# Kernel tuning notes

Measured on AMD Instinct MI355X. Metric: run time of the kernel, lower is better.

## Reference

```python
import jax, jax.numpy as jnp
import numpy as np
from jax import lax

DIM = 512
HEADS = 8
N = 2048
B = 4
EPS = 1e-12  # torch F.normalize eps


def setup_inputs() -> dict:
    key = jax.random.key(0)
    ks = jax.random.split(key, 8)
    s = 0.02
    return {
        "x": jax.random.normal(ks[0], (B, DIM, N), jnp.float32),
        "w_qkv": jax.random.normal(ks[1], (3 * DIM, DIM, 1), jnp.float32) * s,
        "b_qkv": jax.random.normal(ks[2], (3 * DIM,), jnp.float32) * s,
        "w_dw": jax.random.normal(ks[3], (3 * DIM, 1, 3), jnp.float32) * s,
        "b_dw": jax.random.normal(ks[4], (3 * DIM,), jnp.float32) * s,
        "w_po": jax.random.normal(ks[5], (DIM, DIM, 1), jnp.float32) * s,
        "b_po": jax.random.normal(ks[6], (DIM,), jnp.float32) * s,
        "temperature": jnp.ones((HEADS, 1, 1), jnp.float32),
    }


def _l2norm(x, axis):
    n = jnp.sqrt(jnp.sum(x * x, axis=axis, keepdims=True))
    return x / jnp.maximum(n, EPS)


def reference(x, w_qkv, b_qkv, w_dw, b_dw, w_po, b_po, temperature):
    b, c, n = x.shape
    ch = c // HEADS
    # 1x1 conv (pointwise)
    qkv = jnp.einsum('oc,bcn->bon', w_qkv[:, :, 0], x) + b_qkv[None, :, None]
    # depthwise conv k=3, pad=1
    qkv = lax.conv_general_dilated(
        qkv, w_dw, window_strides=(1,), padding=[(1, 1)],
        dimension_numbers=('NCH', 'OIH', 'NCH'),
        feature_group_count=3 * c) + b_dw[None, :, None]
    q, k, v = jnp.split(qkv, 3, axis=1)  # each [b, c, n]
    q = q.reshape(b, HEADS, ch, n)
    k = k.reshape(b, HEADS, ch, n)
    v = v.reshape(b, HEADS, ch, n)
    q = _l2norm(q, axis=-1)          # normalize over sequence axis
    k = _l2norm(k, axis=1)           # normalize over HEAD axis (faithful)
    # attn[i, j] = sum_c k[c, i] * q[c, j]  -> [b, h, n, n]
    attn = jnp.einsum('bhci,bhcj->bhij', k, q) * temperature[None]
    attn = jax.nn.softmax(attn, axis=-1)
    out = jnp.einsum('bhij,bhcj->bhic', attn, v)  # [b, h, n, ch]
    out = out.transpose(0, 1, 3, 2).reshape(b, c, n)  # b (head c) n
    out = jnp.einsum('oc,bcn->bon', w_po[:, :, 0], out) + b_po[None, :, None]
    return out
```

## Files before the change

kernel.cpp:

```cpp
#include <hip/hip_runtime.h>
#include <hip/hip_bf16.h>

#define BATCH 4
#define DIM 512
#define HEADS 8
#define CH 64
#define SEQ 2048
#define C3 1536
#define L2EPS 1e-12f

typedef float f32x4 __attribute__((ext_vector_type(4)));
typedef short s16x8 __attribute__((ext_vector_type(8)));
typedef unsigned short ushort_t;

static __device__ __forceinline__ unsigned bfpair(float a, float b) {
  unsigned ua = __builtin_bit_cast(unsigned, a);
  unsigned ub = __builtin_bit_cast(unsigned, b);
  ua = (ua + 0x7FFFu + ((ua >> 16) & 1u)) >> 16;
  ub = (ub + 0x7FFFu + ((ub >> 16) & 1u)) >> 16;
  return ua | (ub << 16);
}

static __device__ __forceinline__ ushort_t bf16r(float a) {
  unsigned u = __builtin_bit_cast(unsigned, a);
  u = (u + 0x7FFFu + ((u >> 16) & 1u)) >> 16;
  return (ushort_t)u;
}

static __device__ __forceinline__ float bf2f(ushort_t u) {
  return __builtin_bit_cast(float, ((unsigned)u) << 16);
}

static __device__ __forceinline__ unsigned cvtpk(float lo, float hi) {
  unsigned r;
  asm("v_cvt_pk_bf16_f32 %0, %1, %2" : "=v"(r) : "v"(lo), "v"(hi));
  return r;
}

static __device__ __forceinline__ float fexp2(float x) {
  float r;
  asm("v_exp_f32 %0, %1" : "=v"(r) : "v"(x));
  return r;
}

static __device__ __forceinline__ void gl_lds16(const void* g, void* l) {
  __builtin_amdgcn_global_load_lds(
      (const __attribute__((address_space(1))) unsigned int*)g,
      (__attribute__((address_space(3))) unsigned int*)l, 16, 0, 0);
}

__global__ __launch_bounds__(256) void prep_inputs(
    const float* __restrict__ x, const float* __restrict__ wq,
    const float* __restrict__ wp, unsigned* __restrict__ xbt,
    unsigned* __restrict__ wqb, unsigned* __restrict__ wpb) {
  __shared__ unsigned T[64][32];
  const int bid = blockIdx.x;
  if (bid < 1024) {
    const int xx = bid & 31, ky = (bid >> 5) & 7, b = bid >> 8;
    const int k0 = ky * 64;
    const int n0 = xx * 64;
    const int nl = threadIdx.x & 63;
    const int dwg = threadIdx.x >> 6;
    const float* xb = x + ((size_t)b * DIM + k0) * SEQ + n0 + nl;
#pragma unroll
    for (int dd = 0; dd < 8; ++dd) {
      const int dw = dwg * 8 + dd;
      const float v0 = xb[(size_t)(2 * dw) * SEQ];
      const float v1 = xb[(size_t)(2 * dw + 1) * SEQ];
      T[nl][dw ^ (4 * (nl & 7))] = bfpair(v0, v1);
    }
    __syncthreads();
#pragma unroll
    for (int rep = 0; rep < 8; ++rep) {
      const int id = rep * 256 + threadIdx.x;
      const int row = id >> 5, dw = id & 31;
      xbt[((size_t)b * SEQ + n0 + row) * 256 + (k0 >> 1) + dw] = T[row][dw];
    }
  } else {
    const int id = (bid - 1024) * 256 + threadIdx.x;
    const float* src;
    unsigned* dst;
    int rid;
    if (id < 1536 * 256) { src = wq; dst = wqb; rid = id; }
    else                 { src = wp; dst = wpb; rid = id - 1536 * 256; }
    const int m = rid >> 8, dcol = rid & 255;
    const int chunk = dcol >> 5, dw = dcol & 31;
    const int sdw = chunk * 32 + (dw ^ (4 * (m & 7)));
    const float* s = src + (size_t)m * 512 + 2 * sdw;
    dst[rid] = bfpair(s[0], s[1]);
  }
}

template <bool OBF, int BM>
__global__ __launch_bounds__(256) void gemm_mfma_bf16(
    const ushort_t* __restrict__ Wb, const ushort_t* __restrict__ Bt,
    const float* __restrict__ bias, float* __restrict__ Y,
    int M, int N) {
  constexpr int AW = BM / 4;
  constexpr int MFR = BM / 32;
  __shared__ __align__(16) char lds[BM * 128 + 16384];
  char* As = lds;
  char* Bs = lds + BM * 128;
  const int b = blockIdx.z;
  const int m0 = blockIdx.y * BM, n0 = blockIdx.x * 128;
  const int t = threadIdx.x, w = t >> 6, lane = t & 63;
  const int l15 = lane & 15, g = lane >> 4;
  const int key = 16 * (l15 & 7);
  const int wm = (w >> 1) * (BM / 2), wn = (w & 1) * 64;

  const int rsub = lane >> 3;
  const int csub = (lane & 7) * 8;

  f32x4 acc[MFR][4] = {};

  const ushort_t* Ag0 = Wb + (size_t)(m0 + AW * w + rsub) * 512 + csub;
  const ushort_t* Bg0 = Bt + ((size_t)b * N + n0 + 32 * w + rsub) * 512 + csub;
  char* Al0 = As + (AW * w) * 128;
  char* Bl0 = Bs + (32 * w) * 128;

  for (int kc = 0; kc < 8; ++kc) {
    const int ko64 = kc * 64;
#pragma unroll
    for (int ri = 0; ri < 4; ++ri) {
      if (ri < AW / 8)
        gl_lds16(Ag0 + (size_t)(8 * ri) * 512 + ko64, Al0 + ri * 1024);
      gl_lds16(Bg0 + (size_t)(8 * ri) * 512 + ko64, Bl0 + ri * 1024);
    }
    __syncthreads();
    const char* Abase = As + (wm + l15) * 128;
    const char* Bbase = Bs + (wn + l15) * 128;
#pragma unroll
    for (int ks = 0; ks < 2; ++ks) {
      const int ko = (64 * ks + 16 * g) ^ key;
      s16x8 af[MFR], bf[4];
#pragma unroll
      for (int mf = 0; mf < MFR; ++mf) af[mf] = *(const s16x8*)(Abase + mf * 2048 + ko);
#pragma unroll
      for (int nf = 0; nf < 4; ++nf) bf[nf] = *(const s16x8*)(Bbase + nf * 2048 + ko);
#pragma unroll
      for (int mf = 0; mf < MFR; ++mf)
#pragma unroll
        for (int nf = 0; nf < 4; ++nf)
          acc[mf][nf] = __builtin_amdgcn_mfma_f32_16x16x32_bf16(
              af[mf], bf[nf], acc[mf][nf], 0, 0, 0);
    }
    __syncthreads();
  }

#pragma unroll
  for (int mf = 0; mf < MFR; ++mf) {
#pragma unroll
    for (int rg = 0; rg < 4; ++rg) {
      const int m = m0 + wm + 16 * mf + 4 * g + rg;
      const float bv = bias[m];
      if constexpr (OBF) {
        ushort_t* yp =
            (ushort_t*)Y + ((size_t)b * M + m) * N + n0 + wn + l15;
#pragma unroll
        for (int nf = 0; nf < 4; ++nf)
          yp[16 * nf] = bf16r(acc[mf][nf][rg] + bv);
      } else {
        float* yp = Y + ((size_t)b * M + m) * N + n0 + wn + l15;
#pragma unroll
        for (int nf = 0; nf < 4; ++nf)
          yp[16 * nf] = acc[mf][nf][rg] + bv;
      }
    }
  }
}

__global__ __launch_bounds__(256) void dwconv2(
    const ushort_t* __restrict__ pre, const float* __restrict__ wdw,
    const float* __restrict__ bdw, ushort_t* __restrict__ qkv,
    unsigned* __restrict__ vb, float* __restrict__ rq) {
  __shared__ float red[4];
  const int row = blockIdx.x;
  const int o = row % C3;
  const int b = row / C3;
  const int n0 = threadIdx.x * 8;
  const ushort_t* src = pre + (size_t)row * SEQ + n0;
  const s16x8 mv = *(const s16x8*)src;
  const float left  = (n0 > 0) ? bf2f(src[-1]) : 0.f;
  const float right = (n0 < SEQ - 8) ? bf2f(src[8]) : 0.f;
  const float w0 = wdw[o * 3 + 0], w1 = wdw[o * 3 + 1], w2 = wdw[o * 3 + 2];
  const float bv = bdw[o];
  float mid[8];
#pragma unroll
  for (int u = 0; u < 8; ++u) mid[u] = bf2f((ushort_t)mv[u]);
  const float lf[8] = {left,   mid[0], mid[1], mid[2],
                       mid[3], mid[4], mid[5], mid[6]};
  const float rt[8] = {mid[1], mid[2], mid[3], mid[4],
                       mid[5], mid[6], mid[7], right};
  float y[8];
#pragma unroll
  for (int u = 0; u < 8; ++u) y[u] = w0 * lf[u] + w1 * mid[u] + w2 * rt[u] + bv;

  if (o < 2 * DIM) {
    uint4 pk;
    pk.x = bfpair(y[0], y[1]); pk.y = bfpair(y[2], y[3]);
    pk.z = bfpair(y[4], y[5]); pk.w = bfpair(y[6], y[7]);
    *(uint4*)(qkv + (size_t)row * SEQ + n0) = pk;
    if (o < DIM) {
      float s = 0.f;
#pragma unroll
      for (int u = 0; u < 8; ++u) s += y[u] * y[u];
#pragma unroll
      for (int off = 32; off > 0; off >>= 1) s += __shfl_down(s, off);
      if ((threadIdx.x & 63) == 0) red[threadIdx.x >> 6] = s;
      __syncthreads();
      if (threadIdx.x == 0) {
        const float tv = red[0] + red[1] + red[2] + red[3];
        rq[b * DIM + o] = 1.0f / fmaxf(sqrtf(tv), L2EPS);
      }
    }
  } else {
    const int oc = o - 2 * DIM;
    const int h = oc >> 6, cc = oc & 63;
    const int bh = b * 8 + h;
    const int jt = n0 >> 6, d0 = (n0 & 63) >> 1;
    uint4 pk;
    pk.x = bfpair(y[0], y[1]); pk.y = bfpair(y[2], y[3]);
    pk.z = bfpair(y[4], y[5]); pk.w = bfpair(y[6], y[7]);
    *(uint4*)&vb[((size_t)(bh * 32 + jt) * 64 + cc) * 32 +
                 (d0 ^ (4 * (cc & 7)))] = pk;
  }
}

__global__ __launch_bounds__(256) void knorm_kernel(
    const ushort_t* __restrict__ qkv, float* __restrict__ rk) {
  const int idx = blockIdx.x * 256 + threadIdx.x;
  const int n = idx & (SEQ - 1);
  const int cc = (idx >> 11) & 63;
  const int b = idx >> 17;
  const ushort_t* base = qkv + ((size_t)b * C3 + DIM + cc) * SEQ + n;
  float s = 0.f;
#pragma unroll
  for (int h = 0; h < HEADS; ++h) {
    float v = bf2f(base[(size_t)h * CH * SEQ]);
    s += v * v;
  }
  rk[idx] = 1.0f / fmaxf(sqrtf(s), L2EPS);
}

__global__ __launch_bounds__(256) void prep2(
    const ushort_t* __restrict__ qkv, const float* __restrict__ rq,
    const float* __restrict__ rk, const float* __restrict__ temp,
    unsigned* __restrict__ qt, unsigned* __restrict__ kt) {
  __shared__ unsigned T[64][32];
  const int jt = blockIdx.x, bh = blockIdx.y, sec = blockIdx.z;
  const int b = bh >> 3, h = bh & 7;
  const int jl = threadIdx.x & 63, dwg = threadIdx.x >> 6;
  const int j = jt * 64 + jl;
  if (sec == 0) {
    const ushort_t* base = qkv + ((size_t)b * C3 + h * CH) * SEQ + j;
    const float* rqb = rq + b * DIM + h * CH;
#pragma unroll
    for (int dd = 0; dd < 8; ++dd) {
      const int dw = dwg * 8 + dd;
      float v0 = bf2f(base[(size_t)(2 * dw) * SEQ]) * rqb[2 * dw];
      float v1 = bf2f(base[(size_t)(2 * dw + 1) * SEQ]) * rqb[2 * dw + 1];
      T[jl][dw ^ (4 * (jl & 7))] = bfpair(v0, v1);
    }
  } else {
    const float f = temp[h] * 1.44269504f;
    const ushort_t* base = qkv + ((size_t)b * C3 + DIM + h * CH) * SEQ + j;
    const float* rkb = rk + (size_t)b * CH * SEQ + j;
#pragma unroll
    for (int dd = 0; dd < 8; ++dd) {
      const int dw = dwg * 8 + dd;
      float v0 = bf2f(base[(size_t)(2 * dw) * SEQ]) *
                 rkb[(size_t)(2 * dw) * SEQ] * f;
      float v1 = bf2f(base[(size_t)(2 * dw + 1) * SEQ]) *
                 rkb[(size_t)(2 * dw + 1) * SEQ] * f;
      T[jl][dw ^ (4 * (jl & 7))] = bfpair(v0, v1);
    }
  }
  __syncthreads();
  unsigned* dst = (sec == 0 ? qt : kt) + ((size_t)bh * SEQ + jt * 64) * 32;
#pragma unroll
  for (int rep = 0; rep < 8; ++rep) {
    const int id = rep * 256 + threadIdx.x;
    const int row = id >> 5, dw = id & 31;
    const unsigned val = T[row][dw ^ (4 * (row & 7))];
    if (sec == 0) {
      const int s = row >> 5, rl = row & 31;
      const int dr = (s << 5) | (16 * ((rl >> 2) & 1) + 4 * (rl >> 3) + (rl & 3));
      dst[dr * 32 + (dw ^ (4 * (dr & 7)))] = val;
    } else {
      dst[row * 32 + dw] = val;
    }
  }
}

__global__ __launch_bounds__(256, 2) void flash_mfma(
    const ushort_t* __restrict__ qt, const ushort_t* __restrict__ kt,
    const ushort_t* __restrict__ vb, unsigned* __restrict__ attn_t) {
  __shared__ __align__(16) char lds[65536];
  char* const QA = lds;
  char* const QB = lds + 16384;
  char* const VA = lds + 32768;
  char* const VB = lds + 49152;

  const int orig = blockIdx.y * 16 + blockIdx.x;
  const int swz = (orig & 7) * 64 + (orig >> 3);
  const int bh = swz >> 4, b = bh >> 3, h = bh & 7;
  const int i0 = (swz & 15) * 128;

  const int t = threadIdx.x, w = t >> 6, lane = t & 63;
  const int l15 = lane & 15, g = lane >> 4;
  const int key = 16 * (lane & 7);

  const ushort_t* ktp =
      kt + ((size_t)bh * SEQ + i0 + 32 * w + l15) * 64 + 8 * g;
  s16x8 kf0[2], kf1[2];
#pragma unroll
  for (int ib = 0; ib < 2; ++ib) {
    kf0[ib] = *(const s16x8*)(ktp + ib * 1024);
    kf1[ib] = *(const s16x8*)(ktp + ib * 1024 + 32);
  }

  const ushort_t* qtile = qt + (size_t)bh * SEQ * 64;
  const ushort_t* vtile = vb + (size_t)bh * 32 * 4096;

  const int li0 = (w * 2) * 64 + lane;
  const int li1 = li0 + 64;
  const int wo = (w * 2) * 1024;

  f32x4 accO[4][2] = {};
  float lr[2] = {};

#define FSTAGE2(JT, QD, VD)                                               \
  do {                                                                    \
    gl_lds16(qtile + (size_t)(JT) * 4096 + li0 * 8, (QD) + wo);           \
    gl_lds16(qtile + (size_t)(JT) * 4096 + li1 * 8, (QD) + wo + 1024);    \
    gl_lds16(qtile + (size_t)(JT + 1) * 4096 + li0 * 8, (QD) + 8192 + wo);\
    gl_lds16(qtile + (size_t)(JT + 1) * 4096 + li1 * 8,                   \
             (QD) + 8192 + wo + 1024);                                    \
    gl_lds16(vtile + (size_t)(JT) * 4096 + li0 * 8, (VD) + wo);           \
    gl_lds16(vtile + (size_t)(JT) * 4096 + li1 * 8, (VD) + wo + 1024);    \
    gl_lds16(vtile + (size_t)(JT + 1) * 4096 + li0 * 8, (VD) + 8192 + wo);\
    gl_lds16(vtile + (size_t)(JT + 1) * 4096 + li1 * 8,                   \
             (VD) + 8192 + wo + 1024);                                    \
  } while (0)

  auto compute = [&](const char* Qs, const char* Vs) {
    s16x8 vf[2][4];
#pragma unroll
    for (int ks = 0; ks < 2; ++ks)
#pragma unroll
      for (int mf = 0; mf < 4; ++mf)
        vf[ks][mf] = *(const s16x8*)(Vs + (16 * mf + l15) * 128 +
                                     ((16 * g + 64 * ks) ^ key));

    f32x4 st[4][2];
    __builtin_amdgcn_s_setprio(1);
#pragma unroll
    for (int jf = 0; jf < 4; ++jf) {
      const char* qrow = Qs + (16 * jf + l15) * 128;
      s16x8 a0 = *(const s16x8*)(qrow + ((16 * g) ^ key));
      s16x8 a1 = *(const s16x8*)(qrow + ((16 * g + 64) ^ key));
#pragma unroll
      for (int ib = 0; ib < 2; ++ib) {
        f32x4 z = {};
        z = __builtin_amdgcn_mfma_f32_16x16x32_bf16(a0, kf0[ib], z, 0, 0, 0);
        z = __builtin_amdgcn_mfma_f32_16x16x32_bf16(a1, kf1[ib], z, 0, 0, 0);
        st[jf][ib] = z;
      }
    }
    __builtin_amdgcn_s_setprio(0);

    s16x8 pb[2][2];
#pragma unroll
    for (int ib = 0; ib < 2; ++ib)
#pragma unroll
      for (int ks = 0; ks < 2; ++ks) {
        const float e0 = fexp2(st[2 * ks][ib][0]);
        const float e1 = fexp2(st[2 * ks][ib][1]);
        const float e2 = fexp2(st[2 * ks][ib][2]);
        const float e3 = fexp2(st[2 * ks][ib][3]);
        const float e4 = fexp2(st[2 * ks + 1][ib][0]);
        const float e5 = fexp2(st[2 * ks + 1][ib][1]);
        const float e6 = fexp2(st[2 * ks + 1][ib][2]);
        const float e7 = fexp2(st[2 * ks + 1][ib][3]);
        lr[ib] += ((e0 + e1) + (e2 + e3)) + ((e4 + e5) + (e6 + e7));
        uint4 u;
        u.x = cvtpk(e0, e1);
        u.y = cvtpk(e2, e3);
        u.z = cvtpk(e4, e5);
        u.w = cvtpk(e6, e7);
        pb[ib][ks] = __builtin_bit_cast(s16x8, u);
      }

    __builtin_amdgcn_s_setprio(1);
#pragma unroll
    for (int ks = 0; ks < 2; ++ks)
#pragma unroll
      for (int mf = 0; mf < 4; ++mf)
#pragma unroll
        for (int ib = 0; ib < 2; ++ib)
          accO[mf][ib] = __builtin_amdgcn_mfma_f32_16x16x32_bf16(
              vf[ks][mf], pb[ib][ks], accO[mf][ib], 0, 0, 0);
    __builtin_amdgcn_s_setprio(0);
  };

  FSTAGE2(0, QA, VA);
  __syncthreads();
#pragma unroll 1
  for (int s = 0; s < 8; ++s) {
    const int t4 = 4 * s;
    FSTAGE2(t4 + 2, QB, VB);
    compute(QA, VA);
    compute(QA + 8192, VA + 8192);
    __syncthreads();
    if (s < 7) FSTAGE2(t4 + 4, QA, VA);
    compute(QB, VB);
    compute(QB + 8192, VB + 8192);
    __syncthreads();
  }

  float inv[2];
#pragma unroll
  for (int ib = 0; ib < 2; ++ib) {
    lr[ib] += __shfl_xor(lr[ib], 16);
    lr[ib] += __shfl_xor(lr[ib], 32);
    inv[ib] = 1.0f / lr[ib];
  }

  unsigned* Pw = (unsigned*)(lds + w * 4096);
  const int kk = 4 * (l15 & 7);
#pragma unroll
  for (int ib = 0; ib < 2; ++ib)
#pragma unroll
    for (int mf = 0; mf < 4; ++mf) {
      uint2 pk;
      pk.x = cvtpk(accO[mf][ib][0] * inv[ib], accO[mf][ib][1] * inv[ib]);
      pk.y = cvtpk(accO[mf][ib][2] * inv[ib], accO[mf][ib][3] * inv[ib]);
      const int dwb = 8 * mf + 2 * g;
      *(uint2*)&Pw[(16 * ib + l15) * 32 + (dwb ^ kk)] = pk;
    }
  __syncthreads();
#pragma unroll
  for (int rep = 0; rep < 16; ++rep) {
    const int id = rep * 64 + lane;
    const int row = id >> 5, dw = id & 31;
    attn_t[((size_t)b * SEQ + i0 + 32 * w + row) * 256 + h * 32 + dw] =
        Pw[row * 32 + dw];
  }
#undef FSTAGE2
}

extern "C" void kernel_launch(void* const* d_in, const int* in_sizes, int n_in,
                              void* d_out, int out_size, void* d_ws, size_t ws_size,
                              hipStream_t stream) {
  const float* x      = (const float*)d_in[0];
  const float* w_qkv  = (const float*)d_in[1];
  const float* b_qkv  = (const float*)d_in[2];
  const float* w_dw   = (const float*)d_in[3];
  const float* b_dw   = (const float*)d_in[4];
  const float* w_po   = (const float*)d_in[5];
  const float* b_po   = (const float*)d_in[6];
  const float* temp   = (const float*)d_in[7];
  float* out = (float*)d_out;
  float* ws  = (float*)d_ws;

  ushort_t* qkv_pre_b = (ushort_t*)ws;
  ushort_t* qkvb = (ushort_t*)(ws + 12582912);
  float* rq      = ws + 25165824;
  float* rk      = ws + 25167872;
  unsigned* xbt  = (unsigned*)(ws + 25692160);
  unsigned* wqb  = (unsigned*)(ws + 27789312);
  unsigned* wpb  = (unsigned*)(ws + 28182528);
  unsigned* vb     = (unsigned*)(ws + 25692160);
  unsigned* qt     = (unsigned*)(ws);
  unsigned* kt     = (unsigned*)(ws + 2097152);
  unsigned* attn_t = (unsigned*)(ws + 4194304);

  prep_inputs<<<3072, 256, 0, stream>>>(x, w_qkv, w_po, xbt, wqb, wpb);

  gemm_mfma_bf16<true, 128>
      <<<dim3(SEQ / 128, C3 / 128, BATCH), 256, 0, stream>>>(
          (const ushort_t*)wqb, (const ushort_t*)xbt, b_qkv,
          (float*)qkv_pre_b, C3, SEQ);

  dwconv2<<<BATCH * C3, 256, 0, stream>>>(qkv_pre_b, w_dw, b_dw, qkvb, vb, rq);

  knorm_kernel<<<(BATCH * CH * SEQ) / 256, 256, 0, stream>>>(qkvb, rk);

  prep2<<<dim3(32, BATCH * HEADS, 2), 256, 0, stream>>>(
      qkvb, rq, rk, temp, qt, kt);

  flash_mfma<<<dim3(SEQ / 128, BATCH * HEADS), 256, 0, stream>>>(
      (const ushort_t*)qt, (const ushort_t*)kt, (const ushort_t*)vb, attn_t);

  gemm_mfma_bf16<false, 64>
      <<<dim3(SEQ / 128, DIM / 64, BATCH), 256, 0, stream>>>(
          (const ushort_t*)wpb, (const ushort_t*)attn_t, b_po, out, DIM, SEQ);
}
```

Before: 102.2 us.

## Recompute depthwise conv on the fly instead of materializing Q/K buffer

The q and k depthwise-conv outputs are no longer written to an intermediate bf16 buffer. The qnorm, knorm and prep2 kernels each recompute the 3-tap conv directly from the pointwise-conv output, and dwconv now handles only V. This removes one write and one read of the q/k intermediate, at the cost of redundant conv arithmetic, extra neighbor loads and an additional kernel launch. The workspace layout is reshuffled so qt/kt no longer alias qkv_pre_b.

```diff
diff --git a/kernel.cpp b/kernel.cpp
--- a/kernel.cpp
+++ b/kernel.cpp
@@ -47,6 +47,14 @@
   __builtin_amdgcn_global_load_lds(
       (const __attribute__((address_space(1))) unsigned int*)g,
       (__attribute__((address_space(3))) unsigned int*)l, 16, 0, 0);
+}
+
+static __device__ __forceinline__ float dconv(
+    const ushort_t* row, int j, float w0, float w1, float w2, float bv) {
+  const float l = (j > 0) ? bf2f(row[j - 1]) : 0.f;
+  const float m = bf2f(row[j]);
+  const float r = (j < SEQ - 1) ? bf2f(row[j + 1]) : 0.f;
+  return w0 * l + w1 * m + w2 * r + bv;
 }
 
 __global__ __launch_bounds__(256) void prep_inputs(
@@ -169,16 +177,15 @@
   }
 }
 
-__global__ __launch_bounds__(256) void dwconv2(
+__global__ __launch_bounds__(256) void dwconv_v(
     const ushort_t* __restrict__ pre, const float* __restrict__ wdw,
-    const float* __restrict__ bdw, ushort_t* __restrict__ qkv,
-    unsigned* __restrict__ vb, float* __restrict__ rq) {
-  __shared__ float red[4];
-  const int row = blockIdx.x;
-  const int o = row % C3;
-  const int b = row / C3;
+    const float* __restrict__ bdw, unsigned* __restrict__ vb) {
+  const int bid = blockIdx.x;
+  const int oc = bid & 511;
+  const int b = bid >> 9;
+  const int o = 2 * DIM + oc;
   const int n0 = threadIdx.x * 8;
-  const ushort_t* src = pre + (size_t)row * SEQ + n0;
+  const ushort_t* src = pre + ((size_t)b * C3 + o) * SEQ + n0;
   const s16x8 mv = *(const s16x8*)src;
   const float left  = (n0 > 0) ? bf2f(src[-1]) : 0.f;
   const float right = (n0 < SEQ - 8) ? bf2f(src[8]) : 0.f;
@@ -195,55 +202,75 @@
 #pragma unroll
   for (int u = 0; u < 8; ++u) y[u] = w0 * lf[u] + w1 * mid[u] + w2 * rt[u] + bv;
 
-  if (o < 2 * DIM) {
-    uint4 pk;
-    pk.x = bfpair(y[0], y[1]); pk.y = bfpair(y[2], y[3]);
-    pk.z = bfpair(y[4], y[5]); pk.w = bfpair(y[6], y[7]);
-    *(uint4*)(qkv + (size_t)row * SEQ + n0) = pk;
-    if (o < DIM) {
-      float s = 0.f;
-#pragma unroll
-      for (int u = 0; u < 8; ++u) s += y[u] * y[u];
-#pragma unroll
-      for (int off = 32; off > 0; off >>= 1) s += __shfl_down(s, off);
-      if ((threadIdx.x & 63) == 0) red[threadIdx.x >> 6] = s;
-      __syncthreads();
-      if (threadIdx.x == 0) {
-        const float tv = red[0] + red[1] + red[2] + red[3];
-        rq[b * DIM + o] = 1.0f / fmaxf(sqrtf(tv), L2EPS);
-      }
-    }
-  } else {
-    const int oc = o - 2 * DIM;
-    const int h = oc >> 6, cc = oc & 63;
-    const int bh = b * 8 + h;
-    const int jt = n0 >> 6, d0 = (n0 & 63) >> 1;
-    uint4 pk;
-    pk.x = bfpair(y[0], y[1]); pk.y = bfpair(y[2], y[3]);
-    pk.z = bfpair(y[4], y[5]); pk.w = bfpair(y[6], y[7]);
-    *(uint4*)&vb[((size_t)(bh * 32 + jt) * 64 + cc) * 32 +
-                 (d0 ^ (4 * (cc & 7)))] = pk;
+  const int h = oc >> 6, cc = oc & 63;
+  const int bh = b * 8 + h;
+  const int jt = n0 >> 6, d0 = (n0 & 63) >> 1;
+  uint4 pk;
+  pk.x = bfpair(y[0], y[1]); pk.y = bfpair(y[2], y[3]);
+  pk.z = bfpair(y[4], y[5]); pk.w = bfpair(y[6], y[7]);
+  *(uint4*)&vb[((size_t)(bh * 32 + jt) * 64 + cc) * 32 +
+               (d0 ^ (4 * (cc & 7)))] = pk;
+}
+
+__global__ __launch_bounds__(256) void qnorm_kernel(
+    const ushort_t* __restrict__ pre, const float* __restrict__ wdw,
+    const float* __restrict__ bdw, float* __restrict__ rq) {
+  __shared__ float red[4];
+  const int bid = blockIdx.x;
+  const int o = bid & (DIM - 1);
+  const int b = bid >> 9;
+  const int n0 = threadIdx.x * 8;
+  const ushort_t* src = pre + ((size_t)b * C3 + o) * SEQ + n0;
+  const s16x8 mv = *(const s16x8*)src;
+  const float left  = (n0 > 0) ? bf2f(src[-1]) : 0.f;
+  const float right = (n0 < SEQ - 8) ? bf2f(src[8]) : 0.f;
+  const float w0 = wdw[o * 3 + 0], w1 = wdw[o * 3 + 1], w2 = wdw[o * 3 + 2];
+  const float bv = bdw[o];
+  float mid[8];
+#pragma unroll
+  for (int u = 0; u < 8; ++u) mid[u] = bf2f((ushort_t)mv[u]);
+  const float lf[8] = {left,   mid[0], mid[1], mid[2],
+                       mid[3], mid[4], mid[5], mid[6]};
+  const float rt[8] = {mid[1], mid[2], mid[3], mid[4],
+                       mid[5], mid[6], mid[7], right};
+  float s = 0.f;
+#pragma unroll
+  for (int u = 0; u < 8; ++u) {
+    const float y = w0 * lf[u] + w1 * mid[u] + w2 * rt[u] + bv;
+    s += y * y;
+  }
+#pragma unroll
+  for (int off = 32; off > 0; off >>= 1) s += __shfl_down(s, off);
+  if ((threadIdx.x & 63) == 0) red[threadIdx.x >> 6] = s;
+  __syncthreads();
+  if (threadIdx.x == 0) {
+    const float tv = red[0] + red[1] + red[2] + red[3];
+    rq[bid] = 1.0f / fmaxf(sqrtf(tv), L2EPS);
   }
 }
 
 __global__ __launch_bounds__(256) void knorm_kernel(
-    const ushort_t* __restrict__ qkv, float* __restrict__ rk) {
+    const ushort_t* __restrict__ pre, const float* __restrict__ wdw,
+    const float* __restrict__ bdw, float* __restrict__ rk) {
   const int idx = blockIdx.x * 256 + threadIdx.x;
   const int n = idx & (SEQ - 1);
   const int cc = (idx >> 11) & 63;
   const int b = idx >> 17;
-  const ushort_t* base = qkv + ((size_t)b * C3 + DIM + cc) * SEQ + n;
   float s = 0.f;
 #pragma unroll
   for (int h = 0; h < HEADS; ++h) {
-    float v = bf2f(base[(size_t)h * CH * SEQ]);
-    s += v * v;
+    const int o = DIM + h * CH + cc;
+    const ushort_t* row = pre + ((size_t)b * C3 + o) * SEQ;
+    const float y = dconv(row, n, wdw[o * 3], wdw[o * 3 + 1],
+                          wdw[o * 3 + 2], bdw[o]);
+    s += y * y;
   }
   rk[idx] = 1.0f / fmaxf(sqrtf(s), L2EPS);
 }
 
 __global__ __launch_bounds__(256) void prep2(
-    const ushort_t* __restrict__ qkv, const float* __restrict__ rq,
+    const ushort_t* __restrict__ pre, const float* __restrict__ wdw,
+    const float* __restrict__ bdw, const float* __restrict__ rq,
     const float* __restrict__ rk, const float* __restrict__ temp,
     unsigned* __restrict__ qt, unsigned* __restrict__ kt) {
   __shared__ unsigned T[64][32];
@@ -252,25 +279,33 @@
   const int jl = threadIdx.x & 63, dwg = threadIdx.x >> 6;
   const int j = jt * 64 + jl;
   if (sec == 0) {
-    const ushort_t* base = qkv + ((size_t)b * C3 + h * CH) * SEQ + j;
     const float* rqb = rq + b * DIM + h * CH;
 #pragma unroll
     for (int dd = 0; dd < 8; ++dd) {
       const int dw = dwg * 8 + dd;
-      float v0 = bf2f(base[(size_t)(2 * dw) * SEQ]) * rqb[2 * dw];
-      float v1 = bf2f(base[(size_t)(2 * dw + 1) * SEQ]) * rqb[2 * dw + 1];
+      const int o0 = h * CH + 2 * dw, o1 = o0 + 1;
+      const ushort_t* r0 = pre + ((size_t)b * C3 + o0) * SEQ;
+      const ushort_t* r1 = pre + ((size_t)b * C3 + o1) * SEQ;
+      float v0 = dconv(r0, j, wdw[o0 * 3], wdw[o0 * 3 + 1],
+                       wdw[o0 * 3 + 2], bdw[o0]) * rqb[2 * dw];
+      float v1 = dconv(r1, j, wdw[o1 * 3], wdw[o1 * 3 + 1],
+                       wdw[o1 * 3 + 2], bdw[o1]) * rqb[2 * dw + 1];
       T[jl][dw ^ (4 * (jl & 7))] = bfpair(v0, v1);
     }
   } else {
     const float f = temp[h] * 1.44269504f;
-    const ushort_t* base = qkv + ((size_t)b * C3 + DIM + h * CH) * SEQ + j;
     const float* rkb = rk + (size_t)b * CH * SEQ + j;
 #pragma unroll
     for (int dd = 0; dd < 8; ++dd) {
       const int dw = dwg * 8 + dd;
-      float v0 = bf2f(base[(size_t)(2 * dw) * SEQ]) *
+      const int o0 = DIM + h * CH + 2 * dw, o1 = o0 + 1;
+      const ushort_t* r0 = pre + ((size_t)b * C3 + o0) * SEQ;
+      const ushort_t* r1 = pre + ((size_t)b * C3 + o1) * SEQ;
+      float v0 = dconv(r0, j, wdw[o0 * 3], wdw[o0 * 3 + 1],
+                       wdw[o0 * 3 + 2], bdw[o0]) *
                  rkb[(size_t)(2 * dw) * SEQ] * f;
-      float v1 = bf2f(base[(size_t)(2 * dw + 1) * SEQ]) *
+      float v1 = dconv(r1, j, wdw[o1 * 3], wdw[o1 * 3 + 1],
+                       wdw[o1 * 3 + 2], bdw[o1]) *
                  rkb[(size_t)(2 * dw + 1) * SEQ] * f;
       T[jl][dw ^ (4 * (jl & 7))] = bfpair(v0, v1);
     }
@@ -464,16 +499,15 @@
   float* ws  = (float*)d_ws;
 
   ushort_t* qkv_pre_b = (ushort_t*)ws;
-  ushort_t* qkvb = (ushort_t*)(ws + 12582912);
+  unsigned* qt     = (unsigned*)(ws + 12582912);
+  unsigned* kt     = (unsigned*)(ws + 14680064);
+  unsigned* attn_t = (unsigned*)(ws + 4194304);
   float* rq      = ws + 25165824;
   float* rk      = ws + 25167872;
   unsigned* xbt  = (unsigned*)(ws + 25692160);
   unsigned* wqb  = (unsigned*)(ws + 27789312);
   unsigned* wpb  = (unsigned*)(ws + 28182528);
-  unsigned* vb     = (unsigned*)(ws + 25692160);
-  unsigned* qt     = (unsigned*)(ws);
-  unsigned* kt     = (unsigned*)(ws + 2097152);
-  unsigned* attn_t = (unsigned*)(ws + 4194304);
+  unsigned* vb   = (unsigned*)(ws + 25692160);
 
   prep_inputs<<<3072, 256, 0, stream>>>(x, w_qkv, w_po, xbt, wqb, wpb);
 
@@ -482,12 +516,14 @@
           (const ushort_t*)wqb, (const ushort_t*)xbt, b_qkv,
           (float*)qkv_pre_b, C3, SEQ);
 
-  dwconv2<<<BATCH * C3, 256, 0, stream>>>(qkv_pre_b, w_dw, b_dw, qkvb, vb, rq);
-
-  knorm_kernel<<<(BATCH * CH * SEQ) / 256, 256, 0, stream>>>(qkvb, rk);
+  dwconv_v<<<BATCH * DIM, 256, 0, stream>>>(qkv_pre_b, w_dw, b_dw, vb);
+
+  qnorm_kernel<<<BATCH * DIM, 256, 0, stream>>>(qkv_pre_b, w_dw, b_dw, rq);
+  knorm_kernel<<<(BATCH * CH * SEQ) / 256, 256, 0, stream>>>(
+      qkv_pre_b, w_dw, b_dw, rk);
 
   prep2<<<dim3(32, BATCH * HEADS, 2), 256, 0, stream>>>(
-      qkvb, rq, rk, temp, qt, kt);
+      qkv_pre_b, w_dw, b_dw, rq, rk, temp, qt, kt);
 
   flash_mfma<<<dim3(SEQ / 128, BATCH * HEADS), 256, 0, stream>>>(
       (const ushort_t*)qt, (const ushort_t*)kt, (const ushort_t*)vb, attn_t);
```

Result: slower. 121.3 us (+18.6%).

## Split flash attention block into 8 waves of 16 rows each

Applied to the files above, without the earlier changes.

The flash attention kernel now runs 512 threads per block, with each wave owning 16 output rows instead of 32. That halves the per-wave accumulator, score and K-fragment registers, and the staging loads and final store are redistributed across all 8 waves. The aim is more resident waves per CU to hide latency. In exchange, every wave re-reads the shared Q/V LDS tiles for fewer rows, which doubles LDS read traffic per MFMA, and barriers now span more waves.

```diff
diff --git a/kernel.cpp b/kernel.cpp
--- a/kernel.cpp
+++ b/kernel.cpp
@@ -292,7 +292,7 @@
   }
 }
 
-__global__ __launch_bounds__(256, 2) void flash_mfma(
+__global__ __launch_bounds__(512, 4) void flash_mfma(
     const ushort_t* __restrict__ qt, const ushort_t* __restrict__ kt,
     const ushort_t* __restrict__ vb, unsigned* __restrict__ attn_t) {
   __shared__ __align__(16) char lds[65536];
@@ -311,36 +311,25 @@
   const int key = 16 * (lane & 7);
 
   const ushort_t* ktp =
-      kt + ((size_t)bh * SEQ + i0 + 32 * w + l15) * 64 + 8 * g;
-  s16x8 kf0[2], kf1[2];
-#pragma unroll
-  for (int ib = 0; ib < 2; ++ib) {
-    kf0[ib] = *(const s16x8*)(ktp + ib * 1024);
-    kf1[ib] = *(const s16x8*)(ktp + ib * 1024 + 32);
-  }
+      kt + ((size_t)bh * SEQ + i0 + 16 * w + l15) * 64 + 8 * g;
+  const s16x8 kf0 = *(const s16x8*)(ktp);
+  const s16x8 kf1 = *(const s16x8*)(ktp + 32);
 
   const ushort_t* qtile = qt + (size_t)bh * SEQ * 64;
   const ushort_t* vtile = vb + (size_t)bh * 32 * 4096;
 
-  const int li0 = (w * 2) * 64 + lane;
-  const int li1 = li0 + 64;
-  const int wo = (w * 2) * 1024;
-
-  f32x4 accO[4][2] = {};
-  float lr[2] = {};
+  const int li = w * 64 + lane;
+  const int wo = w * 1024;
+
+  f32x4 accO[4] = {};
+  float lr = 0.f;
 
 #define FSTAGE2(JT, QD, VD)                                               \
   do {                                                                    \
-    gl_lds16(qtile + (size_t)(JT) * 4096 + li0 * 8, (QD) + wo);           \
-    gl_lds16(qtile + (size_t)(JT) * 4096 + li1 * 8, (QD) + wo + 1024);    \
-    gl_lds16(qtile + (size_t)(JT + 1) * 4096 + li0 * 8, (QD) + 8192 + wo);\
-    gl_lds16(qtile + (size_t)(JT + 1) * 4096 + li1 * 8,                   \
-             (QD) + 8192 + wo + 1024);                                    \
-    gl_lds16(vtile + (size_t)(JT) * 4096 + li0 * 8, (VD) + wo);           \
-    gl_lds16(vtile + (size_t)(JT) * 4096 + li1 * 8, (VD) + wo + 1024);    \
-    gl_lds16(vtile + (size_t)(JT + 1) * 4096 + li0 * 8, (VD) + 8192 + wo);\
-    gl_lds16(vtile + (size_t)(JT + 1) * 4096 + li1 * 8,                   \
-             (VD) + 8192 + wo + 1024);                                    \
+    gl_lds16(qtile + (size_t)(JT) * 4096 + li * 8, (QD) + wo);            \
+    gl_lds16(qtile + (size_t)(JT + 1) * 4096 + li * 8, (QD) + 8192 + wo); \
+    gl_lds16(vtile + (size_t)(JT) * 4096 + li * 8, (VD) + wo);            \
+    gl_lds16(vtile + (size_t)(JT + 1) * 4096 + li * 8, (VD) + 8192 + wo); \
   } while (0)
 
   auto compute = [&](const char* Qs, const char* Vs) {
@@ -352,54 +341,47 @@
         vf[ks][mf] = *(const s16x8*)(Vs + (16 * mf + l15) * 128 +
                                      ((16 * g + 64 * ks) ^ key));
 
-    f32x4 st[4][2];
+    f32x4 st[4];
     __builtin_amdgcn_s_setprio(1);
 #pragma unroll
     for (int jf = 0; jf < 4; ++jf) {
       const char* qrow = Qs + (16 * jf + l15) * 128;
       s16x8 a0 = *(const s16x8*)(qrow + ((16 * g) ^ key));
       s16x8 a1 = *(const s16x8*)(qrow + ((16 * g + 64) ^ key));
-#pragma unroll
-      for (int ib = 0; ib < 2; ++ib) {
-        f32x4 z = {};
-        z = __builtin_amdgcn_mfma_f32_16x16x32_bf16(a0, kf0[ib], z, 0, 0, 0);
-        z = __builtin_amdgcn_mfma_f32_16x16x32_bf16(a1, kf1[ib], z, 0, 0, 0);
-        st[jf][ib] = z;
-      }
+      f32x4 z = {};
+      z = __builtin_amdgcn_mfma_f32_16x16x32_bf16(a0, kf0, z, 0, 0, 0);
+      z = __builtin_amdgcn_mfma_f32_16x16x32_bf16(a1, kf1, z, 0, 0, 0);
+      st[jf] = z;
     }
     __builtin_amdgcn_s_setprio(0);
 
-    s16x8 pb[2][2];
-#pragma unroll
-    for (int ib = 0; ib < 2; ++ib)
-#pragma unroll
-      for (int ks = 0; ks < 2; ++ks) {
-        const float e0 = fexp2(st[2 * ks][ib][0]);
-        const float e1 = fexp2(st[2 * ks][ib][1]);
-        const float e2 = fexp2(st[2 * ks][ib][2]);
-        const float e3 = fexp2(st[2 * ks][ib][3]);
-        const float e4 = fexp2(st[2 * ks + 1][ib][0]);
-        const float e5 = fexp2(st[2 * ks + 1][ib][1]);
-        const float e6 = fexp2(st[2 * ks + 1][ib][2]);
-        const float e7 = fexp2(st[2 * ks + 1][ib][3]);
-        lr[ib] += ((e0 + e1) + (e2 + e3)) + ((e4 + e5) + (e6 + e7));
-        uint4 u;
-        u.x = cvtpk(e0, e1);
-        u.y = cvtpk(e2, e3);
-        u.z = cvtpk(e4, e5);
-        u.w = cvtpk(e6, e7);
-        pb[ib][ks] = __builtin_bit_cast(s16x8, u);
-      }
+    s16x8 pb[2];
+#pragma unroll
+    for (int ks = 0; ks < 2; ++ks) {
+      const float e0 = fexp2(st[2 * ks][0]);
+      const float e1 = fexp2(st[2 * ks][1]);
+      const float e2 = fexp2(st[2 * ks][2]);
+      const float e3 = fexp2(st[2 * ks][3]);
+      const float e4 = fexp2(st[2 * ks + 1][0]);
+      const float e5 = fexp2(st[2 * ks + 1][1]);
+      const float e6 = fexp2(st[2 * ks + 1][2]);
+      const float e7 = fexp2(st[2 * ks + 1][3]);
+      lr += ((e0 + e1) + (e2 + e3)) + ((e4 + e5) + (e6 + e7));
+      uint4 u;
+      u.x = cvtpk(e0, e1);
+      u.y = cvtpk(e2, e3);
+      u.z = cvtpk(e4, e5);
+      u.w = cvtpk(e6, e7);
+      pb[ks] = __builtin_bit_cast(s16x8, u);
+    }
 
     __builtin_amdgcn_s_setprio(1);
 #pragma unroll
     for (int ks = 0; ks < 2; ++ks)
 #pragma unroll
       for (int mf = 0; mf < 4; ++mf)
-#pragma unroll
-        for (int ib = 0; ib < 2; ++ib)
-          accO[mf][ib] = __builtin_amdgcn_mfma_f32_16x16x32_bf16(
-              vf[ks][mf], pb[ib][ks], accO[mf][ib], 0, 0, 0);
+        accO[mf] = __builtin_amdgcn_mfma_f32_16x16x32_bf16(
+            vf[ks][mf], pb[ks], accO[mf], 0, 0, 0);
     __builtin_amdgcn_s_setprio(0);
   };
 
@@ -418,33 +400,28 @@
     __syncthreads();
   }
 
-  float inv[2];
-#pragma unroll
-  for (int ib = 0; ib < 2; ++ib) {
-    lr[ib] += __shfl_xor(lr[ib], 16);
-    lr[ib] += __shfl_xor(lr[ib], 32);
-    inv[ib] = 1.0f / lr[ib];
-  }
-
-  unsigned* Pw = (unsigned*)(lds + w * 4096);
+  lr += __shfl_xor(lr, 16);
+  lr += __shfl_xor(lr, 32);
+  const float inv = 1.0f / lr;
+
+  unsigned* Pw = (unsigned*)(lds + w * 2048);
   const int kk = 4 * (l15 & 7);
 #pragma unroll
-  for (int ib = 0; ib < 2; ++ib)
-#pragma unroll
-    for (int mf = 0; mf < 4; ++mf) {
-      uint2 pk;
-      pk.x = cvtpk(accO[mf][ib][0] * inv[ib], accO[mf][ib][1] * inv[ib]);
-      pk.y = cvtpk(accO[mf][ib][2] * inv[ib], accO[mf][ib][3] * inv[ib]);
-      const int dwb = 8 * mf + 2 * g;
-      *(uint2*)&Pw[(16 * ib + l15) * 32 + (dwb ^ kk)] = pk;
-    }
+  for (int mf = 0; mf < 4; ++mf) {
+    uint2 pk;
+    pk.x = cvtpk(accO[mf][0] * inv, accO[mf][1] * inv);
+    pk.y = cvtpk(accO[mf][2] * inv, accO[mf][3] * inv);
+    const int dwb = 8 * mf + 2 * g;
+    *(uint2*)&Pw[l15 * 32 + (dwb ^ kk)] = pk;
+  }
   __syncthreads();
-#pragma unroll
-  for (int rep = 0; rep < 16; ++rep) {
-    const int id = rep * 64 + lane;
+  const unsigned* Pall = (const unsigned*)lds;
+#pragma unroll
+  for (int rep = 0; rep < 8; ++rep) {
+    const int id = rep * 512 + t;
     const int row = id >> 5, dw = id & 31;
-    attn_t[((size_t)b * SEQ + i0 + 32 * w + row) * 256 + h * 32 + dw] =
-        Pw[row * 32 + dw];
+    attn_t[((size_t)b * SEQ + i0 + row) * 256 + h * 32 + dw] =
+        Pall[row * 32 + dw];
   }
 #undef FSTAGE2
 }
@@ -489,7 +466,7 @@
   prep2<<<dim3(32, BATCH * HEADS, 2), 256, 0, stream>>>(
       qkvb, rq, rk, temp, qt, kt);
 
-  flash_mfma<<<dim3(SEQ / 128, BATCH * HEADS), 256, 0, stream>>>(
+  flash_mfma<<<dim3(SEQ / 128, BATCH * HEADS), 512, 0, stream>>>(
       (const ushort_t*)qt, (const ushort_t*)kt, (const ushort_t*)vb, attn_t);
 
   gemm_mfma_bf16<false, 64>
```

Measured after the change: 102.7 us. About the same (+0.5%).

## Split flash attention over key halves with 512-thread blocks and add merge kernel

Applied to the files above, without the earlier changes.

The flash kernel now runs 512-thread blocks covering 256 query rows, and splits the key/value sequence into two halves along a new grid dimension. Each half writes unnormalized fp32 partial outputs and row sums to workspace. A new attn_finish kernel adds the halves, normalizes, and writes the bf16 transposed attention output. The output projection GEMM also gains a BN template parameter and runs with 64x64 tiles to launch more blocks. This raises parallelism and occupancy, at the cost of an extra launch and fp32 partial-result traffic through global memory.

```diff
diff --git a/kernel.cpp b/kernel.cpp
--- a/kernel.cpp
+++ b/kernel.cpp
@@ -91,32 +91,34 @@
   }
 }
 
-template <bool OBF, int BM>
+template <bool OBF, int BM, int BN>
 __global__ __launch_bounds__(256) void gemm_mfma_bf16(
     const ushort_t* __restrict__ Wb, const ushort_t* __restrict__ Bt,
     const float* __restrict__ bias, float* __restrict__ Y,
     int M, int N) {
   constexpr int AW = BM / 4;
+  constexpr int BW = BN / 4;
   constexpr int MFR = BM / 32;
-  __shared__ __align__(16) char lds[BM * 128 + 16384];
+  constexpr int NFR = BN / 32;
+  __shared__ __align__(16) char lds[(BM + BN) * 128];
   char* As = lds;
   char* Bs = lds + BM * 128;
   const int b = blockIdx.z;
-  const int m0 = blockIdx.y * BM, n0 = blockIdx.x * 128;
+  const int m0 = blockIdx.y * BM, n0 = blockIdx.x * BN;
   const int t = threadIdx.x, w = t >> 6, lane = t & 63;
   const int l15 = lane & 15, g = lane >> 4;
   const int key = 16 * (l15 & 7);
-  const int wm = (w >> 1) * (BM / 2), wn = (w & 1) * 64;
+  const int wm = (w >> 1) * (BM / 2), wn = (w & 1) * (BN / 2);
 
   const int rsub = lane >> 3;
   const int csub = (lane & 7) * 8;
 
-  f32x4 acc[MFR][4] = {};
+  f32x4 acc[MFR][NFR] = {};
 
   const ushort_t* Ag0 = Wb + (size_t)(m0 + AW * w + rsub) * 512 + csub;
-  const ushort_t* Bg0 = Bt + ((size_t)b * N + n0 + 32 * w + rsub) * 512 + csub;
+  const ushort_t* Bg0 = Bt + ((size_t)b * N + n0 + BW * w + rsub) * 512 + csub;
   char* Al0 = As + (AW * w) * 128;
-  char* Bl0 = Bs + (32 * w) * 128;
+  char* Bl0 = Bs + (BW * w) * 128;
 
   for (int kc = 0; kc < 8; ++kc) {
     const int ko64 = kc * 64;
@@ -124,7 +126,8 @@
     for (int ri = 0; ri < 4; ++ri) {
       if (ri < AW / 8)
         gl_lds16(Ag0 + (size_t)(8 * ri) * 512 + ko64, Al0 + ri * 1024);
-      gl_lds16(Bg0 + (size_t)(8 * ri) * 512 + ko64, Bl0 + ri * 1024);
+      if (ri < BW / 8)
+        gl_lds16(Bg0 + (size_t)(8 * ri) * 512 + ko64, Bl0 + ri * 1024);
     }
     __syncthreads();
     const char* Abase = As + (wm + l15) * 128;
@@ -132,15 +135,15 @@
 #pragma unroll
     for (int ks = 0; ks < 2; ++ks) {
       const int ko = (64 * ks + 16 * g) ^ key;
-      s16x8 af[MFR], bf[4];
+      s16x8 af[MFR], bf[NFR];
 #pragma unroll
       for (int mf = 0; mf < MFR; ++mf) af[mf] = *(const s16x8*)(Abase + mf * 2048 + ko);
 #pragma unroll
-      for (int nf = 0; nf < 4; ++nf) bf[nf] = *(const s16x8*)(Bbase + nf * 2048 + ko);
+      for (int nf = 0; nf < NFR; ++nf) bf[nf] = *(const s16x8*)(Bbase + nf * 2048 + ko);
 #pragma unroll
       for (int mf = 0; mf < MFR; ++mf)
 #pragma unroll
-        for (int nf = 0; nf < 4; ++nf)
+        for (int nf = 0; nf < NFR; ++nf)
           acc[mf][nf] = __builtin_amdgcn_mfma_f32_16x16x32_bf16(
               af[mf], bf[nf], acc[mf][nf], 0, 0, 0);
     }
@@ -157,12 +160,12 @@
         ushort_t* yp =
             (ushort_t*)Y + ((size_t)b * M + m) * N + n0 + wn + l15;
 #pragma unroll
-        for (int nf = 0; nf < 4; ++nf)
+        for (int nf = 0; nf < NFR; ++nf)
           yp[16 * nf] = bf16r(acc[mf][nf][rg] + bv);
       } else {
         float* yp = Y + ((size_t)b * M + m) * N + n0 + wn + l15;
 #pragma unroll
-        for (int nf = 0; nf < 4; ++nf)
+        for (int nf = 0; nf < NFR; ++nf)
           yp[16 * nf] = acc[mf][nf][rg] + bv;
       }
     }
@@ -292,19 +295,21 @@
   }
 }
 
-__global__ __launch_bounds__(256, 2) void flash_mfma(
+__global__ __launch_bounds__(512, 4) void flash_mfma(
     const ushort_t* __restrict__ qt, const ushort_t* __restrict__ kt,
-    const ushort_t* __restrict__ vb, unsigned* __restrict__ attn_t) {
+    const ushort_t* __restrict__ vb, float* __restrict__ partO,
+    float* __restrict__ lrpart) {
   __shared__ __align__(16) char lds[65536];
   char* const QA = lds;
   char* const QB = lds + 16384;
   char* const VA = lds + 32768;
   char* const VB = lds + 49152;
 
-  const int orig = blockIdx.y * 16 + blockIdx.x;
-  const int swz = (orig & 7) * 64 + (orig >> 3);
-  const int bh = swz >> 4, b = bh >> 3, h = bh & 7;
-  const int i0 = (swz & 15) * 128;
+  const int orig = blockIdx.y * 8 + blockIdx.x;
+  const int swz = (orig & 7) * 32 + (orig >> 3);
+  const int bh = swz >> 3;
+  const int i0 = (swz & 7) * 256;
+  const int jhalf = blockIdx.z;
 
   const int t = threadIdx.x, w = t >> 6, lane = t & 63;
   const int l15 = lane & 15, g = lane >> 4;
@@ -322,25 +327,18 @@
   const ushort_t* qtile = qt + (size_t)bh * SEQ * 64;
   const ushort_t* vtile = vb + (size_t)bh * 32 * 4096;
 
-  const int li0 = (w * 2) * 64 + lane;
-  const int li1 = li0 + 64;
-  const int wo = (w * 2) * 1024;
+  const int li = t;
+  const int wo = w * 1024;
 
   f32x4 accO[4][2] = {};
   float lr[2] = {};
 
 #define FSTAGE2(JT, QD, VD)                                               \
   do {                                                                    \
-    gl_lds16(qtile + (size_t)(JT) * 4096 + li0 * 8, (QD) + wo);           \
-    gl_lds16(qtile + (size_t)(JT) * 4096 + li1 * 8, (QD) + wo + 1024);    \
-    gl_lds16(qtile + (size_t)(JT + 1) * 4096 + li0 * 8, (QD) + 8192 + wo);\
-    gl_lds16(qtile + (size_t)(JT + 1) * 4096 + li1 * 8,                   \
-             (QD) + 8192 + wo + 1024);                                    \
-    gl_lds16(vtile + (size_t)(JT) * 4096 + li0 * 8, (VD) + wo);           \
-    gl_lds16(vtile + (size_t)(JT) * 4096 + li1 * 8, (VD) + wo + 1024);    \
-    gl_lds16(vtile + (size_t)(JT + 1) * 4096 + li0 * 8, (VD) + 8192 + wo);\
-    gl_lds16(vtile + (size_t)(JT + 1) * 4096 + li1 * 8,                   \
-             (VD) + 8192 + wo + 1024);                                    \
+    gl_lds16(qtile + (size_t)(JT) * 4096 + li * 8, (QD) + wo);            \
+    gl_lds16(qtile + (size_t)(JT + 1) * 4096 + li * 8, (QD) + 8192 + wo); \
+    gl_lds16(vtile + (size_t)(JT) * 4096 + li * 8, (VD) + wo);            \
+    gl_lds16(vtile + (size_t)(JT + 1) * 4096 + li * 8, (VD) + 8192 + wo); \
   } while (0)
 
   auto compute = [&](const char* Qs, const char* Vs) {
@@ -403,50 +401,78 @@
     __builtin_amdgcn_s_setprio(0);
   };
 
-  FSTAGE2(0, QA, VA);
+  const int j0 = jhalf * 16;
+  FSTAGE2(j0, QA, VA);
   __syncthreads();
 #pragma unroll 1
-  for (int s = 0; s < 8; ++s) {
-    const int t4 = 4 * s;
+  for (int s = 0; s < 4; ++s) {
+    const int t4 = j0 + 4 * s;
     FSTAGE2(t4 + 2, QB, VB);
     compute(QA, VA);
     compute(QA + 8192, VA + 8192);
     __syncthreads();
-    if (s < 7) FSTAGE2(t4 + 4, QA, VA);
+    if (s < 3) FSTAGE2(t4 + 4, QA, VA);
     compute(QB, VB);
     compute(QB + 8192, VB + 8192);
     __syncthreads();
   }
 
-  float inv[2];
 #pragma unroll
   for (int ib = 0; ib < 2; ++ib) {
     lr[ib] += __shfl_xor(lr[ib], 16);
     lr[ib] += __shfl_xor(lr[ib], 32);
-    inv[ib] = 1.0f / lr[ib];
-  }
-
-  unsigned* Pw = (unsigned*)(lds + w * 4096);
+  }
+
+  const size_t pid = (size_t)orig * 2 + jhalf;
+  lrpart[(pid * 2 + 0) * 512 + t] = lr[0];
+  lrpart[(pid * 2 + 1) * 512 + t] = lr[1];
+  f32x4* pop = (f32x4*)partO;
+#pragma unroll
+  for (int mf = 0; mf < 4; ++mf)
+#pragma unroll
+    for (int ib = 0; ib < 2; ++ib)
+      pop[(pid * 8 + mf * 2 + ib) * 512 + t] = accO[mf][ib];
+#undef FSTAGE2
+}
+
+__global__ __launch_bounds__(512) void attn_finish(
+    const float* __restrict__ partO, const float* __restrict__ lrpart,
+    unsigned* __restrict__ attn_t) {
+  __shared__ unsigned Pw[256 * 32];
+  const int r = blockIdx.x;
+  const int swz = (r & 7) * 32 + (r >> 3);
+  const int bh = swz >> 3, b = bh >> 3, h = bh & 7;
+  const int i0 = (swz & 7) * 256;
+  const int t = threadIdx.x, w = t >> 6, lane = t & 63;
+  const int l15 = lane & 15, g = lane >> 4;
   const int kk = 4 * (l15 & 7);
-#pragma unroll
-  for (int ib = 0; ib < 2; ++ib)
+  const f32x4* pop = (const f32x4*)partO;
+  const size_t p0 = (size_t)(r * 2) * 8, p1 = (size_t)(r * 2 + 1) * 8;
+#pragma unroll
+  for (int ib = 0; ib < 2; ++ib) {
+    const float l0 = lrpart[((size_t)(r * 2 + 0) * 2 + ib) * 512 + t];
+    const float l1 = lrpart[((size_t)(r * 2 + 1) * 2 + ib) * 512 + t];
+    const float inv = 1.0f / (l0 + l1);
+    const int orow = 32 * w + 16 * ib + l15;
 #pragma unroll
     for (int mf = 0; mf < 4; ++mf) {
+      const f32x4 a = pop[(p0 + mf * 2 + ib) * 512 + t] +
+                      pop[(p1 + mf * 2 + ib) * 512 + t];
       uint2 pk;
-      pk.x = cvtpk(accO[mf][ib][0] * inv[ib], accO[mf][ib][1] * inv[ib]);
-      pk.y = cvtpk(accO[mf][ib][2] * inv[ib], accO[mf][ib][3] * inv[ib]);
+      pk.x = cvtpk(a[0] * inv, a[1] * inv);
+      pk.y = cvtpk(a[2] * inv, a[3] * inv);
       const int dwb = 8 * mf + 2 * g;
-      *(uint2*)&Pw[(16 * ib + l15) * 32 + (dwb ^ kk)] = pk;
-    }
+      *(uint2*)&Pw[orow * 32 + (dwb ^ kk)] = pk;
+    }
+  }
   __syncthreads();
 #pragma unroll
   for (int rep = 0; rep < 16; ++rep) {
-    const int id = rep * 64 + lane;
+    const int id = rep * 512 + t;
     const int row = id >> 5, dw = id & 31;
-    attn_t[((size_t)b * SEQ + i0 + 32 * w + row) * 256 + h * 32 + dw] =
+    attn_t[((size_t)b * SEQ + i0 + row) * 256 + h * 32 + dw] =
         Pw[row * 32 + dw];
   }
-#undef FSTAGE2
 }
 
 extern "C" void kernel_launch(void* const* d_in, const int* in_sizes, int n_in,
@@ -474,10 +500,12 @@
   unsigned* qt     = (unsigned*)(ws);
   unsigned* kt     = (unsigned*)(ws + 2097152);
   unsigned* attn_t = (unsigned*)(ws + 4194304);
+  float* partO  = ws + 12582912;
+  float* lrpart = ws + 20971520;
 
   prep_inputs<<<3072, 256, 0, stream>>>(x, w_qkv, w_po, xbt, wqb, wpb);
 
-  gemm_mfma_bf16<true, 128>
+  gemm_mfma_bf16<true, 128, 128>
       <<<dim3(SEQ / 128, C3 / 128, BATCH), 256, 0, stream>>>(
           (const ushort_t*)wqb, (const ushort_t*)xbt, b_qkv,
           (float*)qkv_pre_b, C3, SEQ);
@@ -489,10 +517,13 @@
   prep2<<<dim3(32, BATCH * HEADS, 2), 256, 0, stream>>>(
       qkvb, rq, rk, temp, qt, kt);
 
-  flash_mfma<<<dim3(SEQ / 128, BATCH * HEADS), 256, 0, stream>>>(
-      (const ushort_t*)qt, (const ushort_t*)kt, (const ushort_t*)vb, attn_t);
-
-  gemm_mfma_bf16<false, 64>
-      <<<dim3(SEQ / 128, DIM / 64, BATCH), 256, 0, stream>>>(
+  flash_mfma<<<dim3(SEQ / 256, BATCH * HEADS, 2), 512, 0, stream>>>(
+      (const ushort_t*)qt, (const ushort_t*)kt, (const ushort_t*)vb,
+      partO, lrpart);
+
+  attn_finish<<<256, 512, 0, stream>>>(partO, lrpart, attn_t);
+
+  gemm_mfma_bf16<false, 64, 64>
+      <<<dim3(SEQ / 64, DIM / 64, BATCH), 256, 0, stream>>>(
           (const ushort_t*)wpb, (const ushort_t*)attn_t, b_po, out, DIM, SEQ);
 }
```

After: 248.4 us. 143% more time.
